# Kernel optimization log

Measured on AMD Instinct MI355X. Metric: run time of the kernel, lower is better.

## Reference

```python
import jax, jax.numpy as jnp
import numpy as np
from jax import lax

B, S, DM = 2, 2048, 2048
H, HKV, D = 16, 4, 128          # heads, kv heads, head_dim = DM // H
CLAMP_MAX = 0.95


def setup_inputs() -> dict:
    key = jax.random.key(0)
    k0, k1, k2, k3 = jax.random.split(key, 4)
    w_scale = 2 ** (-2.5) * (6.0 / (DM + DM)) ** 0.5  # xavier_uniform gain 2^-2.5 scale
    return {
        "hidden_states": jax.random.normal(k0, (B, S, DM), dtype=jnp.float32),
        "Wq": jax.random.uniform(k1, (DM, DM), jnp.float32, -w_scale, w_scale),
        "bq": jnp.zeros((DM,), jnp.float32),
        "Wk": jax.random.uniform(k2, (HKV * D, DM), jnp.float32, -w_scale, w_scale),
        "bk": jnp.zeros((HKV * D,), jnp.float32),
        "Wv": jax.random.uniform(k3, (HKV * D, DM), jnp.float32, -w_scale, w_scale),
        "bv": jnp.zeros((HKV * D,), jnp.float32),
    }


def _gla_forward(hidden_states, Wq, bq, Wk, bk, Wv, bv):
    b, s, _ = hidden_states.shape
    q = hidden_states @ Wq.T + bq                      # [b, s, H*D]
    k = hidden_states @ Wk.T + bk                      # [b, s, HKV*D]
    v = hidden_states @ Wv.T + bv                      # [b, s, HKV*D]
    q = q.reshape(b, s, H, D).transpose(0, 2, 1, 3)    # [b, H, s, D]
    k = k.reshape(b, s, HKV, D).transpose(0, 2, 1, 3)  # [b, HKV, s, D]
    v = v.reshape(b, s, HKV, D).transpose(0, 2, 1, 3)
    rep = H // HKV                                     # repeat_kv (GQA)
    k = jnp.repeat(k, rep, axis=1)                     # [b, H, s, D]
    v = jnp.repeat(v, rep, axis=1)
    q = jax.nn.relu(q)                                 # q_feature_map
    # layer_idx == 0 gate path: k = clamp(sigmoid(k), max=0.95); g = log(1 - k)
    kf = jnp.minimum(jax.nn.sigmoid(k.astype(jnp.float32)), CLAMP_MAX)
    g = jnp.log1p(-kf)                                 # log-space decay, g <= log(0.05) < 0 ... 0
    k = kf.astype(v.dtype)
    scale = D ** -0.5                                  # fla gla default scale = head_dim**-0.5
    q = (q * scale).astype(v.dtype)

    # GLA recurrence over time: S_t = exp(g_t)[:,None] * S_{t-1} + k_t^T v_t ; o_t = q_t S_t
    qs = q.transpose(2, 0, 1, 3)   # [s, b, H, D]
    ks = k.transpose(2, 0, 1, 3)
    vs = v.transpose(2, 0, 1, 3)
    gs = g.transpose(2, 0, 1, 3)

    def step(state, inp):           # state: [b, H, D, D] (key_dim x value_dim)
        qt, kt, vt, gt = inp
        state = state * jnp.exp(gt)[..., :, None] + kt[..., :, None] * vt[..., None, :]
        ot = jnp.einsum('bhd,bhde->bhe', qt, state)
        return state, ot

    S0 = jnp.zeros((b, H, D, D), jnp.float32)
    _, o = lax.scan(step, S0, (qs, ks, vs, gs))        # o: [s, b, H, D]
    o = o.transpose(1, 0, 2, 3).reshape(b, s, H * D)   # 'b h l d -> b l (h d)'
    return o


def reference(hidden_states, Wq, bq, Wk, bk, Wv, bv):
    return _gla_forward(hidden_states, Wq, bq, Wk, bk, Wv, bv)
```

## Files before the change

### kernel.cpp

```cpp
#include <hip/hip_runtime.h>
#include <math.h>

#define B_ 2
#define S_ 2048
#define DM_ 2048
#define H_ 16
#define HKV_ 4
#define D_ 128
#define NKV_ 512
#define M_ 4096
#define CHK_ 32
#define NC_ 64
#define SCALE_ 0.08838834764831845f
#define CLAMP_ 0.95f

typedef unsigned short u16;
typedef u16 ushortx8 __attribute__((ext_vector_type(8)));
typedef __bf16 bf16x8 __attribute__((ext_vector_type(8)));
typedef float f32x4 __attribute__((ext_vector_type(4)));

#define ASYNC16(gsrc, ldst) \
  __builtin_amdgcn_global_load_lds((const __attribute__((address_space(1))) void*)(gsrc), \
                                   (__attribute__((address_space(3))) void*)(ldst), 16, 0, 0)
#define SBAR()    __builtin_amdgcn_s_barrier()
#define WAITV(n)  asm volatile("s_waitcnt vmcnt(" #n ")" ::: "memory")

__device__ __forceinline__ u16 f2b(float x){
  unsigned u = __float_as_uint(x);
  return (u16)((u + 0x7FFFu + ((u >> 16) & 1u)) >> 16);
}
__device__ __forceinline__ float b2f(u16 h){
  return __uint_as_float(((unsigned)h) << 16);
}
__device__ __forceinline__ bf16x8 ld8(const u16* p){
  return __builtin_bit_cast(bf16x8, *(const ushortx8*)p);
}
__device__ __forceinline__ f32x4 mfma16(bf16x8 a, bf16x8 b, f32x4 c){
  return __builtin_amdgcn_mfma_f32_16x16x32_bf16(a, b, c, 0, 0, 0);
}
__device__ __forceinline__ bf16x8 scale8(bf16x8 v, const float* s){
  ushortx8 u = __builtin_bit_cast(ushortx8, v);
  ushortx8 o;
  #pragma unroll
  for (int j = 0; j < 8; ++j) o[j] = f2b(b2f(u[j]) * s[j]);
  return __builtin_bit_cast(bf16x8, o);
}

__global__ void k_cvt_all(const float* __restrict__ hs, const float* __restrict__ Wq,
                          const float* __restrict__ Wk, const float* __restrict__ Wv,
                          u16* __restrict__ hsb, u16* __restrict__ wcb){
  int i = blockIdx.x * blockDim.x + threadIdx.x;
  const float* src; u16* dst;
  if (i < 1048576)      { src = hs + (size_t)i * 8;               dst = hsb + (size_t)i * 8; }
  else if (i < 1572864) { int j = i - 1048576; src = Wq + (size_t)j * 8; dst = wcb + (size_t)j * 8; }
  else if (i < 1703936) { int j = i - 1572864; src = Wk + (size_t)j * 8; dst = wcb + 4194304 + (size_t)j * 8; }
  else                  { int j = i - 1703936; src = Wv + (size_t)j * 8; dst = wcb + 5242880 + (size_t)j * 8; }
  const float4* p = (const float4*)src;
  float4 a = p[0], c = p[1];
  ushortx8 o;
  o[0]=f2b(a.x); o[1]=f2b(a.y); o[2]=f2b(a.z); o[3]=f2b(a.w);
  o[4]=f2b(c.x); o[5]=f2b(c.y); o[6]=f2b(c.z); o[7]=f2b(c.w);
  *(ushortx8*)dst = o;
}

__launch_bounds__(256, 2)
__global__ void k_gemm(const u16* __restrict__ A, const u16* __restrict__ W,
                       const float* __restrict__ bq, const float* __restrict__ bk,
                       const float* __restrict__ bv,
                       u16* __restrict__ qp, u16* __restrict__ kp,
                       float* __restrict__ gG, u16* __restrict__ vT){
  __shared__ u16 L[3 * 8192];
  const int tid = threadIdx.x;
  const int wid = tid >> 6, lane = tid & 63;
  const int m0 = blockIdx.y * 128, n0 = blockIdx.x * 128;
  const int wr = (wid >> 1) * 64, wc = (wid & 1) * 64;
  const int lr = lane & 15;

  int offA[4], offB[4];
  #pragma unroll
  for (int m = 0; m < 4; ++m)
    offA[m] = (wr + m * 16 + lr) * 32 + (((lane >> 4) ^ (lr & 3)) << 3);
  #pragma unroll
  for (int n = 0; n < 4; ++n)
    offB[n] = (wc + n * 16 + lr) * 32 + (((lane >> 4) ^ (lr & 3)) << 3);

  const int srow = wid * 32 + (lane >> 2);
  const int scol = (((lane & 3) ^ ((lane >> 2) & 3)) << 3);
  const u16* gA = A + (size_t)(m0 + srow) * DM_ + scol;
  const u16* gW = W + (size_t)(n0 + srow) * DM_ + scol;
  const int fo = wid * 1024;

#define STG(db, kk0) \
  ASYNC16(gA + (kk0),             L + (db) + fo); \
  ASYNC16(gA + 16 * DM_ + (kk0),  L + (db) + fo + 512); \
  ASYNC16(gW + (kk0),             L + (db) + 4096 + fo); \
  ASYNC16(gW + 16 * DM_ + (kk0),  L + (db) + 4096 + fo + 512)

  f32x4 acc[4][4] = {};

  STG(0, 0);
  STG(8192, 32);

  int sl_cur = 0, sl_st = 16384;
  for (int kt = 0; kt < 64; ++kt){
    WAITV(4);
    SBAR();
    const int k2 = ((kt + 2 < 64) ? kt + 2 : 63) * 32;
    STG(sl_st, k2);
    bf16x8 af[4], bfv[4];
    #pragma unroll
    for (int m = 0; m < 4; ++m) af[m]  = ld8(L + sl_cur + offA[m]);
    #pragma unroll
    for (int n = 0; n < 4; ++n) bfv[n] = ld8(L + sl_cur + 4096 + offB[n]);
    #pragma unroll
    for (int m = 0; m < 4; ++m)
      #pragma unroll
      for (int n = 0; n < 4; ++n)
        acc[m][n] = mfma16(af[m], bfv[n], acc[m][n]);
    sl_cur = (sl_cur == 16384) ? 0 : sl_cur + 8192;
    sl_st  = (sl_st  == 16384) ? 0 : sl_st  + 8192;
  }
#undef STG

  const int lg4 = lane >> 4;
  const int tn = blockIdx.x;
  if (tn < 16){
    #pragma unroll
    for (int i = 0; i < 4; ++i){
      const int rb = m0 + wr + i*16 + lg4*4;
      #pragma unroll
      for (int j = 0; j < 4; ++j){
        const int col = n0 + wc + j*16 + lr;
        const float bb = bq[col];
        #pragma unroll
        for (int r = 0; r < 4; ++r){
          float q = fmaxf(acc[i][j][r] + bb, 0.f) * SCALE_;
          qp[(size_t)(rb + r) * DM_ + col] = f2b(q);
        }
      }
    }
  } else if (tn < 20){
    #pragma unroll
    for (int i = 0; i < 4; ++i){
      const int rb = m0 + wr + i*16 + lg4*4;
      #pragma unroll
      for (int j = 0; j < 4; ++j){
        const int cc = n0 - DM_ + wc + j*16 + lr;
        const float bb = bk[cc];
        #pragma unroll
        for (int r = 0; r < 4; ++r){
          float x = acc[i][j][r] + bb;
          float kf = fminf(1.f / (1.f + __expf(-x)), CLAMP_);
          kp[(size_t)(rb + r) * NKV_ + cc] = f2b(kf);
          gG[(size_t)(rb + r) * NKV_ + cc] = log1pf(-kf);
        }
      }
    }
  } else {
    #pragma unroll
    for (int i = 0; i < 4; ++i){
      const int rb = m0 + wr + i*16 + lg4*4;
      const int bb_ = rb >> 11;
      const int srw = rb & 2047;
      #pragma unroll
      for (int j = 0; j < 4; ++j){
        const int cc = n0 - DM_ - NKV_ + wc + j*16 + lr;
        const float bias = bv[cc];
        const int kv = cc >> 7, e = cc & 127;
        ushort4 pk;
        pk.x = f2b(acc[i][j][0] + bias);
        pk.y = f2b(acc[i][j][1] + bias);
        pk.z = f2b(acc[i][j][2] + bias);
        pk.w = f2b(acc[i][j][3] + bias);
        *(ushort4*)(vT + (((size_t)(bb_ * HKV_ + kv) * D_ + e) * S_ + srw)) = pk;
      }
    }
  }
}

__global__ void k_cumsum(float* __restrict__ g, float* __restrict__ dec){
  const int c = blockIdx.x, b = blockIdx.z;
  const int col = blockIdx.y * 256 + threadIdx.x;
  const size_t base = ((size_t)b * S_ + (size_t)c * CHK_) * NKV_ + col;
  float v[CHK_];
  #pragma unroll
  for (int t = 0; t < CHK_; ++t) v[t] = g[base + (size_t)t * NKV_];
  float acc = 0.f;
  #pragma unroll
  for (int t = 0; t < CHK_; ++t){ acc += v[t]; v[t] = acc; }
  #pragma unroll
  for (int t = 0; t < CHK_; ++t) g[base + (size_t)t * NKV_] = v[t];
  const int kv = col >> 7, d = col & 127;
  dec[(((size_t)b * HKV_ + kv) * NC_ + c) * D_ + d] = __expf(acc);
}

__launch_bounds__(256, 2)
__global__ void k_dstate(const u16* __restrict__ kp, const float* __restrict__ G,
                         const u16* __restrict__ vT, u16* __restrict__ SSt){
  __shared__ float kex[CHK_][D_];
  __shared__ float vl[D_][CHK_ + 1];
  const int c = blockIdx.x, kv = blockIdx.y, b = blockIdx.z;
  const int tid = threadIdx.x;
  const int s0 = c * CHK_;
  const size_t gbase = ((size_t)b * S_ + s0) * NKV_ + kv * D_;
  for (int idx = tid; idx < CHK_ * D_; idx += 256){
    const int t = idx >> 7, d = idx & 127;
    const float Gt  = G[gbase + (size_t)t  * NKV_ + d];
    const float G31 = G[gbase + (size_t)31 * NKV_ + d];
    const float kf = b2f(kp[gbase + (size_t)t * NKV_ + d]);
    kex[t][d] = kf * __expf(G31 - Gt);
  }
  const size_t vbase = ((size_t)(b * HKV_ + kv) * D_) * S_ + s0;
  for (int idx = tid; idx < 512; idx += 256){
    const int e = idx >> 2, t8 = (idx & 3) * 8;
    ushortx8 vv = *(const ushortx8*)(vT + vbase + (size_t)e * S_ + t8);
    #pragma unroll
    for (int u = 0; u < 8; ++u) vl[e][t8 + u] = b2f(vv[u]);
  }
  __syncthreads();
  const int w = tid >> 6, lane = tid & 63;
  const int e = (w & 1) * 64 + lane;
  const int d0 = (w >> 1) * 64;
  float acc[64];
  #pragma unroll
  for (int i = 0; i < 64; ++i) acc[i] = 0.f;
  for (int t = 0; t < CHK_; ++t){
    const float vv = vl[e][t];
    const float4* kr = (const float4*)(&kex[t][d0]);
    #pragma unroll
    for (int i4 = 0; i4 < 16; ++i4){
      float4 kk = kr[i4];
      acc[i4*4+0] = fmaf(vv, kk.x, acc[i4*4+0]);
      acc[i4*4+1] = fmaf(vv, kk.y, acc[i4*4+1]);
      acc[i4*4+2] = fmaf(vv, kk.z, acc[i4*4+2]);
      acc[i4*4+3] = fmaf(vv, kk.w, acc[i4*4+3]);
    }
  }
  const size_t ob = (((size_t)(b * HKV_ + kv) * NC_ + c) * D_ + e) * D_ + d0;
  #pragma unroll
  for (int i8 = 0; i8 < 8; ++i8){
    ushortx8 o;
    #pragma unroll
    for (int u = 0; u < 8; ++u) o[u] = f2b(acc[i8*8 + u]);
    *(ushortx8*)(SSt + ob + i8*8) = o;
  }
}

__global__ void k_scan(u16* __restrict__ SSt, const float* __restrict__ dec){
  const int eg = blockIdx.x, kv = blockIdx.y, b = blockIdx.z;
  const int tid = threadIdx.x;
  const int e = eg * 4 + (tid >> 5);
  const int d4 = (tid & 31) * 4;
  const size_t base  = ((size_t)(b * HKV_ + kv) * NC_) * D_ * D_ + (size_t)e * D_ + d4;
  const size_t dbase = ((size_t)(b * HKV_ + kv) * NC_) * D_ + d4;
  float s0 = 0.f, s1 = 0.f, s2 = 0.f, s3 = 0.f;
  #pragma unroll 4
  for (int c = 0; c < NC_; ++c){
    const size_t off = base + (size_t)c * (D_ * D_);
    ushort4 dv = *(ushort4*)(SSt + off);
    float4 dc = *(const float4*)(dec + dbase + (size_t)c * D_);
    ushort4 wr;
    wr.x = f2b(s0); wr.y = f2b(s1); wr.z = f2b(s2); wr.w = f2b(s3);
    *(ushort4*)(SSt + off) = wr;
    s0 = s0 * dc.x + b2f(dv.x);
    s1 = s1 * dc.y + b2f(dv.y);
    s2 = s2 * dc.z + b2f(dv.z);
    s3 = s3 * dc.w + b2f(dv.w);
  }
}

#define L_SB   0
#define L_QEF  16384
#define L_KE1  32768
#define L_SF   36864
#define LDS_OUT2_BYTES ((36864 + 256) * 2)
__global__ void __launch_bounds__(512)
k_out2(const u16* __restrict__ qp, const u16* __restrict__ kp,
       const float* __restrict__ G, const u16* __restrict__ vT,
       const u16* __restrict__ SSt, float* __restrict__ out){
  extern __shared__ u16 lds[];
  float* sFf = (float*)(lds + L_SF);
  const int c = blockIdx.x, kv = blockIdx.y, b = blockIdx.z;
  const int tid = threadIdx.x, wid = tid >> 6, lane = tid & 63;
  const int hh = wid >> 1, sub = wid & 1;
  const int s0 = c * CHK_;
  const int lr = lane & 15, lk = (lane >> 4) * 8;
  const size_t gb = ((size_t)b * S_ + s0) * NKV_ + kv * D_;
  const size_t qb0 = ((size_t)b * S_ + s0) * DM_ + (kv * 4) * D_;
  const size_t vb = ((size_t)(b * HKV_ + kv) * D_) * S_ + s0;

  {
    const u16* src = SSt + (((size_t)(b * HKV_ + kv) * NC_ + c) * (D_ * D_));
    #pragma unroll
    for (int is = 0; is < 4; ++is){
      const int fo = is * 4096 + wid * 512;
      ASYNC16(src + fo + lane * 8, lds + L_SB + fo);
    }
  }
  const int dmy = tid & 127;
  const float G15v = G[gb + (size_t)15 * NKV_ + dmy];
  if (tid < 128) sFf[tid] = __expf(-G15v);

  for (int idx = tid; idx < 32 * 128; idx += 512){
    const int t = idx >> 7;
    const float Gt = G[gb + (size_t)t * NKV_ + dmy];
    const float kf = b2f(kp[gb + (size_t)t * NKV_ + dmy]);
    const float eGt = __expf(Gt);
    float qv[4];
    #pragma unroll
    for (int q4 = 0; q4 < 4; ++q4) qv[q4] = b2f(qp[qb0 + (size_t)t * DM_ + q4 * D_ + dmy]);
    #pragma unroll
    for (int q4 = 0; q4 < 4; ++q4) lds[L_QEF + q4 * 4096 + idx] = f2b(qv[q4] * eGt);
    lds[L_KE1 + idx] = f2b(kf * __expf(G15v - Gt));
  }
  __syncthreads();

  float sreg[4][8];
  #pragma unroll
  for (int kd = 0; kd < 4; ++kd)
    #pragma unroll
    for (int j = 0; j < 8; ++j) sreg[kd][j] = sFf[kd * 32 + lk + j];

  const u16* QeF = lds + L_QEF + hh * 4096;
  const u16* KE1 = lds + L_KE1;
  f32x4 aU = {}, aL = {}, aO = {};
  if (sub == 0){
    #pragma unroll
    for (int kd = 0; kd < 4; ++kd){
      bf16x8 faU = ld8(&QeF[lr * 128 + kd * 32 + lk]);
      bf16x8 fbU = scale8(ld8(&KE1[lr * 128 + kd * 32 + lk]), sreg[kd]);
      aU = mfma16(faU, fbU, aU);
      bf16x8 faL = scale8(ld8(&QeF[(16 + lr) * 128 + kd * 32 + lk]), sreg[kd]);
      bf16x8 fbL = ld8(&KE1[(16 + lr) * 128 + kd * 32 + lk]);
      aL = mfma16(faL, fbL, aL);
    }
  } else {
    #pragma unroll
    for (int kd = 0; kd < 4; ++kd){
      bf16x8 fa = scale8(ld8(&QeF[(16 + lr) * 128 + kd * 32 + lk]), sreg[kd]);
      bf16x8 fb = ld8(&KE1[lr * 128 + kd * 32 + lk]);
      aO = mfma16(fa, fb, aO);
    }
  }
  __syncthreads();

  u16* Am = lds + L_KE1 + hh * 1024;
  if (sub == 0){
    #pragma unroll
    for (int r = 0; r < 4; ++r){
      const int rr = (lane >> 4) * 4 + r;
      float vU = aU[r]; if (lr > rr) vU = 0.f;
      Am[rr * 32 + lr] = f2b(vU);
      float vL = aL[r]; if (lr > rr) vL = 0.f;
      Am[(16 + rr) * 32 + 16 + lr] = f2b(vL);
    }
  } else {
    #pragma unroll
    for (int r = 0; r < 4; ++r){
      const int rr = (lane >> 4) * 4 + r;
      Am[(16 + rr) * 32 + lr] = f2b(aO[r]);
    }
    for (int i = lane; i < 256; i += 64) Am[(i >> 4) * 32 + 16 + (i & 15)] = 0;
  }
  __syncthreads();

  f32x4 o4[2][4] = {};
  const int ew = sub * 64;
  #pragma unroll
  for (int kd = 0; kd < 4; ++kd){
    bf16x8 fa0 = ld8(&QeF[(0  + lr) * 128 + kd * 32 + lk]);
    bf16x8 fa1 = ld8(&QeF[(16 + lr) * 128 + kd * 32 + lk]);
    #pragma unroll
    for (int j2 = 0; j2 < 4; ++j2){
      bf16x8 fb = ld8(&lds[L_SB + (ew + j2 * 16 + lr) * 128 + kd * 32 + lk]);
      o4[0][j2] = mfma16(fa0, fb, o4[0][j2]);
      o4[1][j2] = mfma16(fa1, fb, o4[1][j2]);
    }
  }
  {
    bf16x8 fa0 = ld8(&Am[lr * 32 + lk]);
    bf16x8 fa1 = ld8(&Am[(16 + lr) * 32 + lk]);
    #pragma unroll
    for (int j2 = 0; j2 < 4; ++j2){
      const u16* vr = vT + vb + (size_t)(ew + j2 * 16 + lr) * S_;
      bf16x8 fb = ld8(vr + lk);
      o4[0][j2] = mfma16(fa0, fb, o4[0][j2]);
      o4[1][j2] = mfma16(fa1, fb, o4[1][j2]);
    }
  }
  const int hD = (kv * 4 + hh) * D_;
  #pragma unroll
  for (int i2 = 0; i2 < 2; ++i2)
    #pragma unroll
    for (int j2 = 0; j2 < 4; ++j2)
      #pragma unroll
      for (int r = 0; r < 4; ++r){
        const int t = i2 * 16 + (lane >> 4) * 4 + r;
        const int e = ew + j2 * 16 + lr;
        out[((size_t)b * S_ + s0 + t) * DM_ + hD + e] = o4[i2][j2][r];
      }
}

extern "C" void kernel_launch(void* const* d_in, const int* in_sizes, int n_in,
                              void* d_out, int out_size, void* d_ws, size_t ws_size,
                              hipStream_t stream){
  const float* hs = (const float*)d_in[0];
  const float* Wq = (const float*)d_in[1];
  const float* bq = (const float*)d_in[2];
  const float* Wk = (const float*)d_in[3];
  const float* bk = (const float*)d_in[4];
  const float* Wv = (const float*)d_in[5];
  const float* bv = (const float*)d_in[6];
  char* ws = (char*)d_ws;
  u16*   hsb = (u16*)(ws);
  u16*   wcb = (u16*)(ws + 16777216);
  u16*   qp  = (u16*)(ws + 29360128);
  u16*   kp  = (u16*)(ws + 46137344);
  float* gG  = (float*)(ws + 50331648);
  u16*   vT  = (u16*)(ws + 58720256);
  float* dec = (float*)(ws + 62914560);
  u16*   SSt = (u16*)(ws + 63176704);
  float* out = (float*)d_out;

  hipFuncSetAttribute((const void*)k_out2,
                      hipFuncAttributeMaxDynamicSharedMemorySize, LDS_OUT2_BYTES);

  k_cvt_all<<<dim3(7168), 256, 0, stream>>>(hs, Wq, Wk, Wv, hsb, wcb);
  k_gemm<<<dim3(24, 32), 256, 0, stream>>>(hsb, wcb, bq, bk, bv, qp, kp, gG, vT);
  k_cumsum<<<dim3(NC_, 2, B_), 256, 0, stream>>>(gG, dec);
  k_dstate<<<dim3(NC_, HKV_, B_), 256, 0, stream>>>(kp, gG, vT, SSt);
  k_scan<<<dim3(32, HKV_, B_), 128, 0, stream>>>(SSt, dec);
  k_out2<<<dim3(NC_, HKV_, B_), 512, LDS_OUT2_BYTES, stream>>>(qp, kp, gG, vT, SSt, out);
}
```

Before: 145.6 us.

## Fuse activation fp32-to-bf16 conversion into GEMM A-tile loading

Removes the separate conversion pass over hidden_states. The GEMM now loads fp32 A tiles into registers, converts them to bf16 with simpler round-half-up rounding, and writes them to LDS. Weights still stream to LDS through async loads. This restructures the pipeline into a three-stage rotation with register double-buffering, which cuts one write and one read of the 16MB bf16 activation copy. In exchange, each GEMM block reads fp32 A twice as wide and on every N tile (24 times), and the rounding mode changes slightly.

```diff
diff --git a/kernel.cpp b/kernel.cpp
--- a/kernel.cpp
+++ b/kernel.cpp
@@ -24,11 +24,15 @@
                                    (__attribute__((address_space(3))) void*)(ldst), 16, 0, 0)
 #define SBAR()    __builtin_amdgcn_s_barrier()
 #define WAITV(n)  asm volatile("s_waitcnt vmcnt(" #n ")" ::: "memory")
+#define LGKM0()   asm volatile("s_waitcnt lgkmcnt(0)" ::: "memory")
 
 __device__ __forceinline__ u16 f2b(float x){
   unsigned u = __float_as_uint(x);
   return (u16)((u + 0x7FFFu + ((u >> 16) & 1u)) >> 16);
 }
+__device__ __forceinline__ u16 f2bu(float x){
+  return (u16)((__float_as_uint(x) + 0x8000u) >> 16);
+}
 __device__ __forceinline__ float b2f(u16 h){
   return __uint_as_float(((unsigned)h) << 16);
 }
@@ -37,6 +41,9 @@
 }
 __device__ __forceinline__ f32x4 mfma16(bf16x8 a, bf16x8 b, f32x4 c){
   return __builtin_amdgcn_mfma_f32_16x16x32_bf16(a, b, c, 0, 0, 0);
+}
+__device__ __forceinline__ ushort4 pk4(float4 f){
+  ushort4 o; o.x = f2bu(f.x); o.y = f2bu(f.y); o.z = f2bu(f.z); o.w = f2bu(f.w); return o;
 }
 __device__ __forceinline__ bf16x8 scale8(bf16x8 v, const float* s){
   ushortx8 u = __builtin_bit_cast(ushortx8, v);
@@ -46,15 +53,13 @@
   return __builtin_bit_cast(bf16x8, o);
 }
 
-__global__ void k_cvt_all(const float* __restrict__ hs, const float* __restrict__ Wq,
-                          const float* __restrict__ Wk, const float* __restrict__ Wv,
-                          u16* __restrict__ hsb, u16* __restrict__ wcb){
+__global__ void k_cvt_w(const float* __restrict__ Wq, const float* __restrict__ Wk,
+                        const float* __restrict__ Wv, u16* __restrict__ wcb){
   int i = blockIdx.x * blockDim.x + threadIdx.x;
   const float* src; u16* dst;
-  if (i < 1048576)      { src = hs + (size_t)i * 8;               dst = hsb + (size_t)i * 8; }
-  else if (i < 1572864) { int j = i - 1048576; src = Wq + (size_t)j * 8; dst = wcb + (size_t)j * 8; }
-  else if (i < 1703936) { int j = i - 1572864; src = Wk + (size_t)j * 8; dst = wcb + 4194304 + (size_t)j * 8; }
-  else                  { int j = i - 1703936; src = Wv + (size_t)j * 8; dst = wcb + 5242880 + (size_t)j * 8; }
+  if (i < 524288)      { src = Wq + (size_t)i * 8;               dst = wcb + (size_t)i * 8; }
+  else if (i < 655360) { int j = i - 524288; src = Wk + (size_t)j * 8; dst = wcb + 4194304 + (size_t)j * 8; }
+  else                 { int j = i - 655360; src = Wv + (size_t)j * 8; dst = wcb + 5242880 + (size_t)j * 8; }
   const float4* p = (const float4*)src;
   float4 a = p[0], c = p[1];
   ushortx8 o;
@@ -64,7 +69,7 @@
 }
 
 __launch_bounds__(256, 2)
-__global__ void k_gemm(const u16* __restrict__ A, const u16* __restrict__ W,
+__global__ void k_gemm(const float* __restrict__ Af, const u16* __restrict__ W,
                        const float* __restrict__ bq, const float* __restrict__ bk,
                        const float* __restrict__ bv,
                        u16* __restrict__ qp, u16* __restrict__ kp,
@@ -74,53 +79,85 @@
   const int wid = tid >> 6, lane = tid & 63;
   const int m0 = blockIdx.y * 128, n0 = blockIdx.x * 128;
   const int wr = (wid >> 1) * 64, wc = (wid & 1) * 64;
-  const int lr = lane & 15;
+  const int lr = lane & 15, lk = (lane >> 4) * 8;
 
   int offA[4], offB[4];
   #pragma unroll
-  for (int m = 0; m < 4; ++m)
-    offA[m] = (wr + m * 16 + lr) * 32 + (((lane >> 4) ^ (lr & 3)) << 3);
-  #pragma unroll
-  for (int n = 0; n < 4; ++n)
-    offB[n] = (wc + n * 16 + lr) * 32 + (((lane >> 4) ^ (lr & 3)) << 3);
-
-  const int srow = wid * 32 + (lane >> 2);
-  const int scol = (((lane & 3) ^ ((lane >> 2) & 3)) << 3);
-  const u16* gA = A + (size_t)(m0 + srow) * DM_ + scol;
-  const u16* gW = W + (size_t)(n0 + srow) * DM_ + scol;
-  const int fo = wid * 1024;
-
-#define STG(db, kk0) \
-  ASYNC16(gA + (kk0),             L + (db) + fo); \
-  ASYNC16(gA + 16 * DM_ + (kk0),  L + (db) + fo + 512); \
-  ASYNC16(gW + (kk0),             L + (db) + 4096 + fo); \
-  ASYNC16(gW + 16 * DM_ + (kk0),  L + (db) + 4096 + fo + 512)
-
+  for (int m = 0; m < 4; ++m) offA[m] = (wr + m * 16 + lr) * 32 + lk;
+  #pragma unroll
+  for (int n = 0; n < 4; ++n) offB[n] = (wc + n * 16 + lr) * 32 + lk;
+
+  const float* gAf = Af + (size_t)(m0 + wid * 32 + (lane >> 3)) * DM_ + (lane & 7) * 4;
+  const int aoff = (wid * 32 + (lane >> 3)) * 32 + (lane & 7) * 4;
+  const u16* gW = W + (size_t)(n0 + wid * 32 + (lane >> 2)) * DM_ + (lane & 3) * 8;
+  const int foW = wid * 1024;
+
+#define LDA(R, kk0) \
+  R##0 = *(const float4*)(gAf + (kk0)); \
+  R##1 = *(const float4*)(gAf +  8 * DM_ + (kk0)); \
+  R##2 = *(const float4*)(gAf + 16 * DM_ + (kk0)); \
+  R##3 = *(const float4*)(gAf + 24 * DM_ + (kk0))
+#define DSW(db, R) { \
+  u16* p_ = L + (db) + aoff; \
+  *(ushort4*)(p_ +   0) = pk4(R##0); \
+  *(ushort4*)(p_ + 256) = pk4(R##1); \
+  *(ushort4*)(p_ + 512) = pk4(R##2); \
+  *(ushort4*)(p_ + 768) = pk4(R##3); }
+#define STGW(db, kk0) \
+  ASYNC16(gW + (kk0),            L + (db) + 4096 + foW); \
+  ASYNC16(gW + 16 * DM_ + (kk0), L + (db) + 4096 + foW + 512)
+
+  float4 rA0, rA1, rA2, rA3, rB0, rB1, rB2, rB3;
   f32x4 acc[4][4] = {};
 
-  STG(0, 0);
-  STG(8192, 32);
-
-  int sl_cur = 0, sl_st = 16384;
-  for (int kt = 0; kt < 64; ++kt){
-    WAITV(4);
-    SBAR();
-    const int k2 = ((kt + 2 < 64) ? kt + 2 : 63) * 32;
-    STG(sl_st, k2);
-    bf16x8 af[4], bfv[4];
-    #pragma unroll
-    for (int m = 0; m < 4; ++m) af[m]  = ld8(L + sl_cur + offA[m]);
-    #pragma unroll
-    for (int n = 0; n < 4; ++n) bfv[n] = ld8(L + sl_cur + 4096 + offB[n]);
-    #pragma unroll
-    for (int m = 0; m < 4; ++m)
-      #pragma unroll
-      for (int n = 0; n < 4; ++n)
-        acc[m][n] = mfma16(af[m], bfv[n], acc[m][n]);
-    sl_cur = (sl_cur == 16384) ? 0 : sl_cur + 8192;
-    sl_st  = (sl_st  == 16384) ? 0 : sl_st  + 8192;
-  }
-#undef STG
+  LDA(rA, 0);
+  STGW(0, 0);
+  LDA(rB, 32);
+  STGW(8192, 32);
+  WAITV(8);
+  DSW(0, rA);
+
+  int sA = 0, sB = 8192, sC = 16384;
+  for (int jj = 0; jj < 32; ++jj){
+    const int j = jj * 2;
+    {
+      WAITV(2); LGKM0(); SBAR();
+      DSW(sB, rB);
+      const int kn = ((j + 2 < 64) ? j + 2 : 63) * 32;
+      LDA(rA, kn);
+      STGW(sC, kn);
+      bf16x8 af[4], bfv[4];
+      #pragma unroll
+      for (int m = 0; m < 4; ++m) af[m]  = ld8(L + sA + offA[m]);
+      #pragma unroll
+      for (int n = 0; n < 4; ++n) bfv[n] = ld8(L + sA + 4096 + offB[n]);
+      #pragma unroll
+      for (int m = 0; m < 4; ++m)
+        #pragma unroll
+        for (int n = 0; n < 4; ++n) acc[m][n] = mfma16(af[m], bfv[n], acc[m][n]);
+      int t = sA; sA = sB; sB = sC; sC = t;
+    }
+    {
+      WAITV(2); LGKM0(); SBAR();
+      DSW(sB, rA);
+      const int kn = ((j + 3 < 64) ? j + 3 : 63) * 32;
+      LDA(rB, kn);
+      STGW(sC, kn);
+      bf16x8 af[4], bfv[4];
+      #pragma unroll
+      for (int m = 0; m < 4; ++m) af[m]  = ld8(L + sA + offA[m]);
+      #pragma unroll
+      for (int n = 0; n < 4; ++n) bfv[n] = ld8(L + sA + 4096 + offB[n]);
+      #pragma unroll
+      for (int m = 0; m < 4; ++m)
+        #pragma unroll
+        for (int n = 0; n < 4; ++n) acc[m][n] = mfma16(af[m], bfv[n], acc[m][n]);
+      int t = sA; sA = sB; sB = sC; sC = t;
+    }
+  }
+#undef LDA
+#undef DSW
+#undef STGW
 
   const int lg4 = lane >> 4;
   const int tn = blockIdx.x;
@@ -337,7 +374,8 @@
   } else {
     #pragma unroll
     for (int kd = 0; kd < 4; ++kd){
-      bf16x8 fa = scale8(ld8(&QeF[(16 + lr) * 128 + kd * 32 + lk]), sreg[kd]);
+      bf16x8 fa = ld8(&QeF[(16 + lr) * 128 + kd * 32 + lk]);
+      fa = scale8(fa, sreg[kd]);
       bf16x8 fb = ld8(&KE1[lr * 128 + kd * 32 + lk]);
       aO = mfma16(fa, fb, aO);
     }
@@ -412,7 +450,6 @@
   const float* Wv = (const float*)d_in[5];
   const float* bv = (const float*)d_in[6];
   char* ws = (char*)d_ws;
-  u16*   hsb = (u16*)(ws);
   u16*   wcb = (u16*)(ws + 16777216);
   u16*   qp  = (u16*)(ws + 29360128);
   u16*   kp  = (u16*)(ws + 46137344);
@@ -425,8 +462,8 @@
   hipFuncSetAttribute((const void*)k_out2,
                       hipFuncAttributeMaxDynamicSharedMemorySize, LDS_OUT2_BYTES);
 
-  k_cvt_all<<<dim3(7168), 256, 0, stream>>>(hs, Wq, Wk, Wv, hsb, wcb);
-  k_gemm<<<dim3(24, 32), 256, 0, stream>>>(hsb, wcb, bq, bk, bv, qp, kp, gG, vT);
+  k_cvt_w<<<dim3(3072), 256, 0, stream>>>(Wq, Wk, Wv, wcb);
+  k_gemm<<<dim3(24, 32), 256, 0, stream>>>(hs, wcb, bq, bk, bv, qp, kp, gG, vT);
   k_cumsum<<<dim3(NC_, 2, B_), 256, 0, stream>>>(gG, dec);
   k_dstate<<<dim3(NC_, HKV_, B_), 256, 0, stream>>>(kp, gG, vT, SSt);
   k_scan<<<dim3(32, HKV_, B_), 128, 0, stream>>>(SSt, dec);
```

Result: slower. 153.8 us (+5.6%).
